# Kernel tuning notes

Measured on AMD Instinct MI355X. Metric: run time of the kernel, lower is better.

The kernel has to match this reference:

```python
import jax, jax.numpy as jnp
import numpy as np

N = 10000
E = 160000
IN_CH, HID, OUT = 14, 128, 4
HEADS = 8
NEG_SLOPE = 0.2


def setup_inputs() -> dict:
    key = jax.random.key(0)
    ks = jax.random.split(key, 16)
    glorot = lambda k, shape: jax.random.normal(k, shape, jnp.float32) * np.sqrt(2.0 / (shape[0] + shape[-1]))
    inp = {
        'x': jax.random.normal(ks[0], (N, IN_CH), jnp.float32),
        'edge_index': jax.random.randint(ks[1], (2, E), 0, N, jnp.int64),
        # layer 1: 14 -> 8 heads x 128, concat
        'W1': glorot(ks[2], (IN_CH, HEADS * HID)),
        'a_src1': glorot(ks[3], (HEADS, HID)),
        'a_dst1': glorot(ks[4], (HEADS, HID)),
        'b1': jnp.zeros((HEADS * HID,), jnp.float32),
        # layer 2: 1024 -> 8 heads x 128, concat
        'W2': glorot(ks[5], (HEADS * HID, HEADS * HID)),
        'a_src2': glorot(ks[6], (HEADS, HID)),
        'a_dst2': glorot(ks[7], (HEADS, HID)),
        'b2': jnp.zeros((HEADS * HID,), jnp.float32),
        # layer 3: 1024 -> 1 head x 4, mean (concat=False)
        'W3': glorot(ks[8], (HEADS * HID, OUT)),
        'a_src3': glorot(ks[9], (1, OUT)),
        'a_dst3': glorot(ks[10], (1, OUT)),
        'b3': jnp.zeros((OUT,), jnp.float32),
    }
    return inp


def gat_conv(x, src, dst, W, a_src, a_dst, b, heads, out_ch, concat):
    n = x.shape[0]
    h = (x @ W).reshape(n, heads, out_ch)                      # [N,H,C]
    al_s = jnp.sum(h * a_src, axis=-1)                         # [N,H]
    al_d = jnp.sum(h * a_dst, axis=-1)                         # [N,H]
    e = al_s[src] + al_d[dst]                                  # [E,H]
    e = jnp.where(e > 0, e, NEG_SLOPE * e)                     # LeakyReLU(0.2)
    # segment softmax over incoming edges of each dst node
    m = jax.ops.segment_max(e, dst, num_segments=n)
    ex = jnp.exp(e - m[dst])
    z = jax.ops.segment_sum(ex, dst, num_segments=n)
    alpha = ex / (z[dst] + 1e-16)                              # [E,H]
    out = jax.ops.segment_sum(h[src] * alpha[:, :, None], dst, num_segments=n)  # [N,H,C]
    out = out.reshape(n, heads * out_ch) if concat else out.mean(axis=1)
    return out + b


def reference(x, edge_index, W1, a_src1, a_dst1, b1, W2, a_src2, a_dst2, b2, W3, a_src3, a_dst3, b3):
    n = x.shape[0]
    # add self-loops (PyG GATConv default)
    loop = jnp.arange(n, dtype=edge_index.dtype)
    src = jnp.concatenate([edge_index[0], loop])
    dst = jnp.concatenate([edge_index[1], loop])
    # dropout layers are identity in eval mode
    h = gat_conv(x, src, dst, W1, a_src1, a_dst1, b1, HEADS, HID, True)
    h = jax.nn.relu(h)
    h = gat_conv(h, src, dst, W2, a_src2, a_dst2, b2, HEADS, HID, True)
    h = jax.nn.relu(h)
    h = gat_conv(h, src, dst, W3, a_src3, a_dst3, b3, 1, OUT, False)
    h = jax.nn.relu(h)
    return h
```

## Files before the change

kernel.cpp:

```cpp
#include <hip/hip_runtime.h>

typedef unsigned short ushort_t;
typedef unsigned int uint32;

#define N_NODES 10000
#define N_EDGES 160000
#define ET (N_NODES + N_EDGES)
#define HT 1024
#define HEADS 8
#define NEG 0.2f

#define O_FLAG     0
#define O_BND      64
#define O_BSUM     192
#define O_COUNTS   512
#define O_OFFS     (O_COUNTS + 40192)
#define O_SSORT    (O_OFFS + 40192)
#define O_ALS1     (O_SSORT + 680192)
#define O_ALD1     (O_ALS1 + 320000)
#define O_ALS2     (O_ALD1 + 320000)
#define O_ALD2     (O_ALS2 + 320000)
#define O_AL3S     O_ALS2
#define O_AL3D     (O_ALS2 + 40192)
#define O_H3       (O_ALS2 + 80384)
#define O_WVEC     (O_ALD2 + 320000)
#define O_W3F      (O_WVEC + 24576)
#define O_S3F      (O_W3F + 16384)
#define O_W2T      (O_S3F + 768)
#define O_BUFA     (O_W2T + 2097152)
#define O_BUFB     (O_BUFA + 20480000)

__device__ __forceinline__ float bf2f(ushort_t u){ return __uint_as_float(((uint32)u) << 16); }
__device__ __forceinline__ ushort_t f2bf(float f){
    uint32 x = __float_as_uint(f);
    return (ushort_t)((x + 0x7fffu + ((x >> 16) & 1u)) >> 16);
}
__device__ __forceinline__ void unpack2(uint32 u, float& lo, float& hi){
    lo = __uint_as_float(u << 16);
    hi = __uint_as_float(u & 0xffff0000u);
}

typedef __bf16 bf16x8 __attribute__((ext_vector_type(8)));
typedef float  f32x4  __attribute__((ext_vector_type(4)));

typedef const __attribute__((address_space(1))) uint32* gas1_u32;
typedef       __attribute__((address_space(3))) uint32* las3_u32;

__device__ __forceinline__ void gload_lds16(const void* g, void* l){
    __builtin_amdgcn_global_load_lds((gas1_u32)g, (las3_u32)l, 16, 0, 0);
}

__device__ __forceinline__ int probe_f32(const uint32* __restrict__ w){
    int cnt = 0;
    for (int i = 0; i < 256; i++){
        uint32 e = (w[i] >> 7) & 0xffu;
        cnt += (e >= 64u && e <= 160u) ? 1 : 0;
    }
    return (cnt > 200) ? 0 : 1;
}
__device__ __forceinline__ int probe_edge64(const int* __restrict__ ei){
    int nz = 0;
    for (int i = 0; i < 128; i++) nz |= ei[2*i + 1];
    return (nz == 0) ? 1 : 0;
}

__device__ __forceinline__ float cvt1(const void* p, int i, int f32){
    return f32 ? ((const float*)p)[i] : bf2f(((const ushort_t*)p)[i]);
}

struct CvtArgs {
    const void* vsrc[6];
    const void* w3src;
    const void* s3src[3];
};

__global__ __launch_bounds__(256) void k_setup(CvtArgs a, const void* __restrict__ W2,
                                               const uint32* __restrict__ w1raw,
                                               const int* __restrict__ eiraw,
                                               int* __restrict__ flags,
                                               float* __restrict__ wvecF, float* __restrict__ W3F,
                                               float* __restrict__ s3F,
                                               int* __restrict__ counts,
                                               float* __restrict__ alS2, float* __restrict__ alD2,
                                               uint32* __restrict__ bnd,
                                               ushort_t* __restrict__ W2T){
    __shared__ ushort_t tile[32][33];
    int b = blockIdx.x, tid = threadIdx.x;
    int f32 = probe_f32(w1raw);
    if (b < 11){
        if (b == 0){
            if (tid < 32) bnd[tid] = 0;
            if (tid == 32) flags[0] = probe_edge64(eiraw);
            if (tid == 33) flags[1] = f32;
        }
        int g = b * 1024 + tid * 4;
        #pragma unroll
        for (int j = 0; j < 4; j++){
            int i = g + j;
            if (i < 6144) wvecF[i] = cvt1(a.vsrc[i >> 10], i & 1023, f32);
            else if (i < 10240) W3F[i - 6144] = cvt1(a.w3src, i - 6144, f32);
            else if (i < 10252){
                int off = i - 10240;
                s3F[(off >> 2) * 16 + (off & 3)] = cvt1(a.s3src[off >> 2], off & 3, f32);
            }
        }
    } else if (b < 21){
        int g = (b - 11) * 1024 + tid * 4;
        #pragma unroll
        for (int j = 0; j < 4; j++) if (g + j < N_NODES) counts[g + j] = 0;
    } else if (b < 178){
        int g = (b - 21) * 1024 + tid * 4;
        if (g < 80000){ *(float4*)(alS2 + g) = make_float4(0,0,0,0); }
        else if (g < 160000){ *(float4*)(alD2 + g - 80000) = make_float4(0,0,0,0); }
    } else {
        int t = b - 178;
        int bx = t & 31, by = t >> 5;
        int cx = tid & 31, ry = (tid >> 5) * 4;
        #pragma unroll
        for (int r = 0; r < 4; r++){
            size_t idx = (size_t)(by*32 + ry + r)*1024 + bx*32 + cx;
            tile[ry + r][cx] = f32 ? f2bf(((const float*)W2)[idx]) : ((const ushort_t*)W2)[idx];
        }
        __syncthreads();
        #pragma unroll
        for (int r = 0; r < 4; r++)
            W2T[(size_t)(bx*32 + ry + r)*1024 + by*32 + cx] = tile[cx][ry + r];
    }
}

__global__ __launch_bounds__(256) void k_exgemm1(const void* __restrict__ ei, const void* __restrict__ x,
                                                 const void* __restrict__ W1, const int* __restrict__ flags,
                                                 const float* __restrict__ wvecF,
                                                 int* __restrict__ counts,
                                                 ushort_t* __restrict__ h1,
                                                 float* __restrict__ alS, float* __restrict__ alD,
                                                 uint32* __restrict__ bnd){
    __shared__ float w1s[14 * HT];
    __shared__ uint32 smax[16];
    int bid = blockIdx.x, tid = threadIdx.x;
    if (bid < 665){
        int i = bid * 256 + tid;
        int is64 = flags[0];
        int d = -1;
        if (i < N_EDGES){
            d = is64 ? (int)((const long long*)ei)[N_EDGES + i] : ((const int*)ei)[N_EDGES + i];
        } else if (i < ET){
            d = i - N_EDGES;
        }
        if (d >= 0) atomicAdd(&counts[d], 1);
        return;
    }
    int gb = bid - 665;
    int f32 = flags[1];
    if (tid < 16) smax[tid] = 0;
    if (f32){
        for (int i = tid * 4; i < 14 * HT; i += 1024)
            *(float4*)(w1s + i) = *(const float4*)((const float*)W1 + i);
    } else {
        for (int i = tid * 4; i < 14 * HT; i += 1024){
            uint2 u = *(const uint2*)((const ushort_t*)W1 + i);
            unpack2(u.x, w1s[i], w1s[i+1]);
            unpack2(u.y, w1s[i+2], w1s[i+3]);
        }
    }
    __syncthreads();
    int c0 = tid * 4;
    float4 sv = *(const float4*)(wvecF + c0);
    float4 dv = *(const float4*)(wvecF + 1024 + c0);
    int head = tid >> 5, l32 = tid & 31;
    #pragma unroll 1
    for (int n = gb; n < N_NODES; n += 512){
        float a0=0.f, a1=0.f, a2=0.f, a3=0.f;
        #pragma unroll
        for (int k = 0; k < 14; k++){
            float xv = f32 ? ((const float*)x)[n*14 + k] : bf2f(((const ushort_t*)x)[n*14 + k]);
            float4 w = *(const float4*)(w1s + k*HT + c0);
            a0 += xv*w.x; a1 += xv*w.y; a2 += xv*w.z; a3 += xv*w.w;
        }
        uint2 o;
        o.x = (uint32)f2bf(a0) | ((uint32)f2bf(a1) << 16);
        o.y = (uint32)f2bf(a2) | ((uint32)f2bf(a3) << 16);
        *(uint2*)(h1 + (size_t)n*HT + c0) = o;
        float h0,h1v,h2,h3v;
        unpack2(o.x, h0, h1v); unpack2(o.y, h2, h3v);
        float s = h0*sv.x + h1v*sv.y + h2*sv.z + h3v*sv.w;
        float d = h0*dv.x + h1v*dv.y + h2*dv.z + h3v*dv.w;
        #pragma unroll
        for (int of = 16; of; of >>= 1){ s += __shfl_xor(s, of, 32); d += __shfl_xor(d, of, 32); }
        if (l32 == 0){
            alS[n*HEADS + head] = s; alD[n*HEADS + head] = d;
            atomicMax(&smax[head],     __float_as_uint(fmaxf(s, 0.f)));
            atomicMax(&smax[8 + head], __float_as_uint(fmaxf(d, 0.f)));
        }
    }
    __syncthreads();
    if (tid < 16) atomicMax(&bnd[tid], smax[tid]);
}

__global__ __launch_bounds__(256) void k_scan_a(const int* __restrict__ counts, int* __restrict__ bsum){
    __shared__ int ws[4];
    int b = blockIdx.x, tid = threadIdx.x;
    int i = b * 256 + tid;
    int v = (i < N_NODES) ? counts[i] : 0;
    int lane = tid & 63, wid = tid >> 6;
    #pragma unroll
    for (int o = 32; o; o >>= 1) v += __shfl_xor(v, o, 64);
    if (lane == 0) ws[wid] = v;
    __syncthreads();
    if (tid == 0) bsum[b] = ws[0] + ws[1] + ws[2] + ws[3];
}

__global__ __launch_bounds__(256) void k_scan_b(int* __restrict__ counts, const int* __restrict__ bsum,
                                                int* __restrict__ offs){
    __shared__ int ws[4];
    int b = blockIdx.x, tid = threadIdx.x;
    int i = b * 256 + tid;
    int v = (i < N_NODES) ? counts[i] : 0;
    int base = 0;
    #pragma unroll 1
    for (int j = 0; j < b; j++) base += bsum[j];
    int lane = tid & 63, wid = tid >> 6;
    int inc = v;
    #pragma unroll
    for (int d = 1; d < 64; d <<= 1){
        int t = __shfl_up(inc, d, 64);
        if (lane >= d) inc += t;
    }
    if (lane == 63) ws[wid] = inc;
    __syncthreads();
    int wpre = 0;
    #pragma unroll
    for (int j = 0; j < 4; j++) if (j < wid) wpre += ws[j];
    int excl = base + wpre + inc - v;
    if (i < N_NODES){ offs[i] = excl; counts[i] = excl; }
    if (i == N_NODES) offs[i] = excl;
}

__global__ __launch_bounds__(256) void k_scatter(const void* __restrict__ ei, const int* __restrict__ flags,
                                                 int* __restrict__ cursors, int* __restrict__ ssort){
    int i = blockIdx.x * 256 + threadIdx.x;
    if (i >= ET) return;
    int is64 = flags[0];
    int s, d;
    if (i < N_EDGES){
        if (is64){
            s = (int)((const long long*)ei)[i];
            d = (int)((const long long*)ei)[N_EDGES + i];
        } else {
            s = ((const int*)ei)[i];
            d = ((const int*)ei)[N_EDGES + i];
        }
    } else { s = i - N_EDGES; d = s; }
    int pos = atomicAdd(&cursors[d], 1);
    ssort[pos] = s;
}

__global__ __launch_bounds__(256) void k_bound(const float* __restrict__ alS2, const float* __restrict__ alD2,
                                               uint32* __restrict__ bnd){
    int g = blockIdx.x * 256 + threadIdx.x;
    int lane = threadIdx.x & 63;
    float ms = 0.f, md = 0.f;
    for (int i = g; i < 80000; i += 10240){ ms = fmaxf(ms, alS2[i]); md = fmaxf(md, alD2[i]); }
    #pragma unroll
    for (int o = 8; o < 64; o <<= 1){
        ms = fmaxf(ms, __shfl_xor(ms, o, 64));
        md = fmaxf(md, __shfl_xor(md, o, 64));
    }
    if (lane < 8){
        atomicMax(&bnd[16 + lane], __float_as_uint(ms));
        atomicMax(&bnd[24 + lane], __float_as_uint(md));
    }
}

__global__ __launch_bounds__(256) void k_gat_agg(const ushort_t* __restrict__ H, const float* __restrict__ alS,
                                                 const float* __restrict__ alD, const uint32* __restrict__ bnd,
                                                 int bo, const int* __restrict__ offs,
                                                 const int* __restrict__ srcs, const float* __restrict__ bias,
                                                 ushort_t* __restrict__ out){
    int tid = threadIdx.x;
    int wv = tid >> 6, lane = tid & 63;
    int n = blockIdx.x * 2 + (wv >> 1);
    int half = wv & 1;
    int beg = offs[n], end = offs[n+1];
    int head = half*4 + (lane >> 4);
    float ad = alD[n*HEADS + head];
    float B = __uint_as_float(bnd[bo + head]) + __uint_as_float(bnd[bo + 8 + head]);

    int ch0 = half*512 + lane*8;
    const ushort_t* Hc = H + ch0;
    float z = 0.f;
    float c0=0.f,c1=0.f,c2=0.f,c3=0.f,c4=0.f,c5=0.f,c6=0.f,c7=0.f;
    for (int c = beg; c < end; c += 64){
        int cn = min(64, end - c);
        int sreg = (lane < cn) ? srcs[c + lane] : 0;
        int j = 0;
        for (; j + 8 <= cn; j += 8){
            int s[8]; uint4 u[8]; float e[8];
            #pragma unroll
            for (int q = 0; q < 8; q++) s[q] = __shfl(sreg, j + q, 64);
            #pragma unroll
            for (int q = 0; q < 8; q++) u[q] = *(const uint4*)(Hc + (size_t)s[q]*HT);
            #pragma unroll
            for (int q = 0; q < 8; q++) e[q] = alS[s[q]*HEADS + head];
            #pragma unroll
            for (int q = 0; q < 8; q++){
                float v = e[q] + ad;
                v = v > 0.f ? v : NEG*v;
                float w = __expf(v - B);
                z += w;
                float f0,f1,f2,f3,f4,f5,f6,f7;
                unpack2(u[q].x,f0,f1); unpack2(u[q].y,f2,f3);
                unpack2(u[q].z,f4,f5); unpack2(u[q].w,f6,f7);
                c0+=w*f0; c1+=w*f1; c2+=w*f2; c3+=w*f3;
                c4+=w*f4; c5+=w*f5; c6+=w*f6; c7+=w*f7;
            }
        }
        for (; j < cn; j++){
            int s0 = __shfl(sreg, j, 64);
            uint4 u0 = *(const uint4*)(Hc + (size_t)s0*HT);
            float v = alS[s0*HEADS + head] + ad;
            v = v > 0.f ? v : NEG*v;
            float w = __expf(v - B);
            z += w;
            float f0,f1,f2,f3,f4,f5,f6,f7;
            unpack2(u0.x,f0,f1); unpack2(u0.y,f2,f3); unpack2(u0.z,f4,f5); unpack2(u0.w,f6,f7);
            c0+=w*f0; c1+=w*f1; c2+=w*f2; c3+=w*f3;
            c4+=w*f4; c5+=w*f5; c6+=w*f6; c7+=w*f7;
        }
    }
    float inv = 1.f / z;
    float4 b0 = *(const float4*)(bias + ch0);
    float4 b1 = *(const float4*)(bias + ch0 + 4);
    c0 = fmaxf(c0*inv + b0.x, 0.f); c1 = fmaxf(c1*inv + b0.y, 0.f);
    c2 = fmaxf(c2*inv + b0.z, 0.f); c3 = fmaxf(c3*inv + b0.w, 0.f);
    c4 = fmaxf(c4*inv + b1.x, 0.f); c5 = fmaxf(c5*inv + b1.y, 0.f);
    c6 = fmaxf(c6*inv + b1.z, 0.f); c7 = fmaxf(c7*inv + b1.w, 0.f);
    uint4 o;
    o.x = (uint32)f2bf(c0) | ((uint32)f2bf(c1) << 16);
    o.y = (uint32)f2bf(c2) | ((uint32)f2bf(c3) << 16);
    o.z = (uint32)f2bf(c4) | ((uint32)f2bf(c5) << 16);
    o.w = (uint32)f2bf(c6) | ((uint32)f2bf(c7) << 16);
    *(uint4*)(out + (size_t)n*HT + ch0) = o;
}

__global__ __launch_bounds__(256) void k_gemm2(const ushort_t* __restrict__ A, const ushort_t* __restrict__ BT,
                                               ushort_t* __restrict__ C,
                                               const float* __restrict__ aS, const float* __restrict__ aD,
                                               float* __restrict__ alS2, float* __restrict__ alD2){
    __shared__ ushort_t lA[128*64];
    __shared__ ushort_t lB[64*64];
    int bn = blockIdx.x, bm = blockIdx.y;
    int tid = threadIdx.x;
    int lane = tid & 63;
    int wave = tid >> 6;
    int wm = wave * 32;
    int lm = lane & 15, kg = lane >> 4;
    int swz = lm & 7;
    f32x4 acc[2][4];
    #pragma unroll
    for (int i = 0; i < 2; i++)
        #pragma unroll
        for (int j = 0; j < 4; j++) acc[i][j] = (f32x4)0.0f;

    int rowA0 = bm * 128, rowB0 = bn * 64;
    for (int k0 = 0; k0 < 1024; k0 += 64){
        #pragma unroll
        for (int it = 0; it < 4; ++it){
            int s = tid + it*256;
            int r = s >> 3, q = s & 7;
            int ra = rowA0 + r; if (ra > N_NODES-1) ra = N_NODES-1;
            gload_lds16(A + (size_t)ra*1024 + k0 + (q ^ (r & 7))*8, lA + s*8);
        }
        #pragma unroll
        for (int it = 0; it < 2; ++it){
            int s = tid + it*256;
            int r = s >> 3, q = s & 7;
            gload_lds16(BT + (size_t)(rowB0 + r)*1024 + k0 + (q ^ (r & 7))*8, lB + s*8);
        }
        __syncthreads();
        #pragma unroll
        for (int kh = 0; kh < 2; kh++){
            bf16x8 af[2], bfr[4];
            int qb = kh*4 + kg;
            int qp = (qb ^ swz) * 8;
            #pragma unroll
            for (int mt = 0; mt < 2; mt++) af[mt]  = *(const bf16x8*)(lA + (wm + mt*16 + lm)*64 + qp);
            #pragma unroll
            for (int nt = 0; nt < 4; nt++) bfr[nt] = *(const bf16x8*)(lB + (nt*16 + lm)*64 + qp);
            #pragma unroll
            for (int mt = 0; mt < 2; mt++)
                #pragma unroll
                for (int nt = 0; nt < 4; nt++)
                    acc[mt][nt] = __builtin_amdgcn_mfma_f32_16x16x32_bf16(af[mt], bfr[nt], acc[mt][nt], 0, 0, 0);
        }
        __syncthreads();
    }
    #pragma unroll
    for (int mt = 0; mt < 2; mt++){
        int row_base = bm*128 + wm + mt*16 + kg*4;
        #pragma unroll
        for (int nt = 0; nt < 4; nt++){
            int col = bn*64 + nt*16 + lm;
            #pragma unroll
            for (int r = 0; r < 4; r++){
                int row = row_base + r;
                if (row < N_NODES) C[(size_t)row*HT + col] = f2bf(acc[mt][nt][r]);
            }
        }
    }
    int head = bn >> 1;
    float as_l[4], ad_l[4];
    #pragma unroll
    for (int nt = 0; nt < 4; nt++){
        as_l[nt] = aS[bn*64 + nt*16 + lm];
        ad_l[nt] = aD[bn*64 + nt*16 + lm];
    }
    #pragma unroll
    for (int mt = 0; mt < 2; mt++){
        #pragma unroll
        for (int r = 0; r < 4; r++){
            float ps = acc[mt][0][r]*as_l[0] + acc[mt][1][r]*as_l[1]
                     + acc[mt][2][r]*as_l[2] + acc[mt][3][r]*as_l[3];
            float pd = acc[mt][0][r]*ad_l[0] + acc[mt][1][r]*ad_l[1]
                     + acc[mt][2][r]*ad_l[2] + acc[mt][3][r]*ad_l[3];
            #pragma unroll
            for (int o = 1; o < 16; o <<= 1){ ps += __shfl_xor(ps, o, 64); pd += __shfl_xor(pd, o, 64); }
            if (lm == 0){
                int row = bm*128 + wm + mt*16 + kg*4 + r;
                if (row < N_NODES){
                    atomicAdd(&alS2[row*HEADS + head], ps);
                    atomicAdd(&alD2[row*HEADS + head], pd);
                }
            }
        }
    }
}

__global__ __launch_bounds__(256) void k_gemm3(const ushort_t* __restrict__ A, const float* __restrict__ W3,
                                               const float* __restrict__ s3,
                                               float* __restrict__ h3, float* __restrict__ al3s, float* __restrict__ al3d){
    int tid = threadIdx.x;
    int lane = tid & 63, wave = tid >> 6;
    int n = blockIdx.x * 4 + wave;
    if (n >= N_NODES) return;
    float4 w3r[16];
    #pragma unroll
    for (int j = 0; j < 16; j++) w3r[j] = ((const float4*)W3)[lane*16 + j];
    const uint4* ap = (const uint4*)(A + (size_t)n*HT + lane*16);
    uint4 u0 = ap[0], u1 = ap[1];
    uint32 uu[8] = {u0.x,u0.y,u0.z,u0.w,u1.x,u1.y,u1.z,u1.w};
    float acc0=0.f, acc1=0.f, acc2=0.f, acc3=0.f;
    #pragma unroll
    for (int p = 0; p < 8; p++){
        float lo, hi;
        unpack2(uu[p], lo, hi);
        float4 wl = w3r[p*2], wh = w3r[p*2+1];
        acc0 += lo*wl.x + hi*wh.x;
        acc1 += lo*wl.y + hi*wh.y;
        acc2 += lo*wl.z + hi*wh.z;
        acc3 += lo*wl.w + hi*wh.w;
    }
    #pragma unroll
    for (int o = 32; o; o >>= 1){
        acc0 += __shfl_xor(acc0, o, 64); acc1 += __shfl_xor(acc1, o, 64);
        acc2 += __shfl_xor(acc2, o, 64); acc3 += __shfl_xor(acc3, o, 64);
    }
    if (lane == 0){
        *(float4*)(h3 + n*4) = make_float4(acc0, acc1, acc2, acc3);
        al3s[n] = acc0*s3[0] + acc1*s3[1] + acc2*s3[2] + acc3*s3[3];
        al3d[n] = acc0*s3[16] + acc1*s3[17] + acc2*s3[18] + acc3*s3[19];
    }
}

__global__ __launch_bounds__(256) void k_gat_agg3(const float* __restrict__ h3, const float* __restrict__ al3s,
                                                  const float* __restrict__ al3d, const int* __restrict__ offs,
                                                  const int* __restrict__ srcs, const float* __restrict__ b3,
                                                  const int* __restrict__ flags, void* __restrict__ out){
    int tid = threadIdx.x;
    int l = tid & 63, wave = tid >> 6;
    int n = blockIdx.x * 4 + wave;
    if (n >= N_NODES) return;
    int beg = offs[n], end = offs[n+1];
    float ad = al3d[n];
    float m = -1e30f;
    for (int e = beg + l; e < end; e += 64){
        float v = al3s[srcs[e]] + ad; v = v > 0.f ? v : NEG*v;
        m = fmaxf(m, v);
    }
    #pragma unroll
    for (int o = 32; o; o >>= 1) m = fmaxf(m, __shfl_xor(m, o, 64));
    float z = 0.f;
    for (int e = beg + l; e < end; e += 64){
        float v = al3s[srcs[e]] + ad; v = v > 0.f ? v : NEG*v;
        z += __expf(v - m);
    }
    #pragma unroll
    for (int o = 32; o; o >>= 1) z += __shfl_xor(z, o, 64);
    float inv = 1.f / (z + 1e-16f);
    float a0=0.f, a1=0.f, a2=0.f, a3=0.f;
    for (int e = beg + l; e < end; e += 64){
        int s = srcs[e];
        float v = al3s[s] + ad; v = v > 0.f ? v : NEG*v;
        float w = __expf(v - m) * inv;
        float4 hv = *(const float4*)(h3 + s*4);
        a0 += w*hv.x; a1 += w*hv.y; a2 += w*hv.z; a3 += w*hv.w;
    }
    #pragma unroll
    for (int o = 32; o; o >>= 1){
        a0 += __shfl_xor(a0, o, 64); a1 += __shfl_xor(a1, o, 64);
        a2 += __shfl_xor(a2, o, 64); a3 += __shfl_xor(a3, o, 64);
    }
    if (l == 0){
        float r0 = fmaxf(a0 + b3[0], 0.f);
        float r1 = fmaxf(a1 + b3[1], 0.f);
        float r2 = fmaxf(a2 + b3[2], 0.f);
        float r3 = fmaxf(a3 + b3[3], 0.f);
        if (flags[1]){
            float* o4 = (float*)out;
            o4[n*4+0]=r0; o4[n*4+1]=r1; o4[n*4+2]=r2; o4[n*4+3]=r3;
        } else {
            ushort_t* o2 = (ushort_t*)out;
            o2[n*4+0]=f2bf(r0); o2[n*4+1]=f2bf(r1); o2[n*4+2]=f2bf(r2); o2[n*4+3]=f2bf(r3);
        }
    }
}

extern "C" void kernel_launch(void* const* d_in, const int* in_sizes, int n_in,
                              void* d_out, int out_size, void* d_ws, size_t ws_size,
                              hipStream_t stream){
    const void* x   = d_in[0];
    const void* ei  = d_in[1];
    const void* W1  = d_in[2];
    const void* W2  = d_in[6];
    const void* W3  = d_in[10];

    char* ws = (char*)d_ws;
    int* flags     = (int*)(ws + O_FLAG);
    uint32* bnd    = (uint32*)(ws + O_BND);
    int* bsum      = (int*)(ws + O_BSUM);
    int* counts    = (int*)(ws + O_COUNTS);
    int* offs      = (int*)(ws + O_OFFS);
    int* ssort     = (int*)(ws + O_SSORT);
    float* alS1    = (float*)(ws + O_ALS1);
    float* alD1    = (float*)(ws + O_ALD1);
    float* alS2    = (float*)(ws + O_ALS2);
    float* alD2    = (float*)(ws + O_ALD2);
    float* al3s    = (float*)(ws + O_AL3S);
    float* al3d    = (float*)(ws + O_AL3D);
    float* h3      = (float*)(ws + O_H3);
    float* wvecF   = (float*)(ws + O_WVEC);
    float* W3F     = (float*)(ws + O_W3F);
    float* s3F     = (float*)(ws + O_S3F);
    ushort_t* W2T  = (ushort_t*)(ws + O_W2T);
    ushort_t* bufA = (ushort_t*)(ws + O_BUFA);
    ushort_t* bufB = (ushort_t*)(ws + O_BUFB);

    const int EB = (ET + 255) / 256;

    CvtArgs ca;
    ca.vsrc[0]=d_in[3];  ca.vsrc[1]=d_in[4];  ca.vsrc[2]=d_in[5];
    ca.vsrc[3]=d_in[7];  ca.vsrc[4]=d_in[8];  ca.vsrc[5]=d_in[9];
    ca.w3src = W3;
    ca.s3src[0]=d_in[11]; ca.s3src[1]=d_in[12]; ca.s3src[2]=d_in[13];

    k_setup<<<1202, 256, 0, stream>>>(ca, W2, (const uint32*)W1, (const int*)ei, flags,
                                      wvecF, W3F, s3F, counts, alS2, alD2, bnd, W2T);
    k_exgemm1<<<1177, 256, 0, stream>>>(ei, x, W1, flags, wvecF, counts, bufA, alS1, alD1, bnd);
    k_scan_a<<<40, 256, 0, stream>>>(counts, bsum);
    k_scan_b<<<40, 256, 0, stream>>>(counts, bsum, offs);
    k_scatter<<<EB, 256, 0, stream>>>(ei, flags, counts, ssort);

    k_gat_agg<<<5000, 256, 0, stream>>>(bufA, alS1, alD1, bnd, 0, offs, ssort, wvecF + 2*1024, bufB);

    k_gemm2<<<dim3(16, 79), 256, 0, stream>>>(bufB, W2T, bufA, wvecF + 3*1024, wvecF + 4*1024, alS2, alD2);
    k_bound<<<40, 256, 0, stream>>>(alS2, alD2, bnd);
    k_gat_agg<<<5000, 256, 0, stream>>>(bufA, alS2, alD2, bnd, 16, offs, ssort, wvecF + 5*1024, bufB);

    k_gemm3<<<2500, 256, 0, stream>>>(bufB, W3F, s3F, h3, al3s, al3d);
    k_gat_agg3<<<2500, 256, 0, stream>>>(h3, al3s, al3d, offs, ssort, s3F + 32, flags, d_out);
}
```

Measured before the change: 335.0 us.

## Shrink setup kernel and merge W2 transpose into the layer-1 mega kernel

The setup kernel is cut down to 12 blocks that only convert the small weight vectors and zero the counts. The W2 transpose and the alS2/alD2 zeroing move into the same launch as the edge counting and the layer-1 GEMM, so that independent work can run concurrently instead of in a serial launch. The W1 shared copy is now stored as bf16 instead of fp32, halving its LDS footprint, which may raise occupancy. The cost is extra unpacking in the inner loop and a heavier, more heterogeneous kernel.

Result: no change. 330.9 us (-1.2%).

```diff
diff --git a/kernel.cpp b/kernel.cpp
--- a/kernel.cpp
+++ b/kernel.cpp
@@ -74,68 +74,49 @@
     const void* s3src[3];
 };
 
-__global__ __launch_bounds__(256) void k_setup(CvtArgs a, const void* __restrict__ W2,
-                                               const uint32* __restrict__ w1raw,
-                                               const int* __restrict__ eiraw,
-                                               int* __restrict__ flags,
-                                               float* __restrict__ wvecF, float* __restrict__ W3F,
-                                               float* __restrict__ s3F,
-                                               int* __restrict__ counts,
-                                               float* __restrict__ alS2, float* __restrict__ alD2,
-                                               uint32* __restrict__ bnd,
-                                               ushort_t* __restrict__ W2T){
-    __shared__ ushort_t tile[32][33];
+__global__ __launch_bounds__(256) void k_pre(CvtArgs a, const uint32* __restrict__ w1raw,
+                                             const int* __restrict__ eiraw,
+                                             int* __restrict__ flags,
+                                             float* __restrict__ wvecF, float* __restrict__ W3F,
+                                             float* __restrict__ s3F,
+                                             int* __restrict__ counts, uint32* __restrict__ bnd){
     int b = blockIdx.x, tid = threadIdx.x;
     int f32 = probe_f32(w1raw);
-    if (b < 11){
-        if (b == 0){
-            if (tid < 32) bnd[tid] = 0;
-            if (tid == 32) flags[0] = probe_edge64(eiraw);
-            if (tid == 33) flags[1] = f32;
-        }
-        int g = b * 1024 + tid * 4;
-        #pragma unroll
-        for (int j = 0; j < 4; j++){
-            int i = g + j;
-            if (i < 6144) wvecF[i] = cvt1(a.vsrc[i >> 10], i & 1023, f32);
-            else if (i < 10240) W3F[i - 6144] = cvt1(a.w3src, i - 6144, f32);
-            else if (i < 10252){
-                int off = i - 10240;
-                s3F[(off >> 2) * 16 + (off & 3)] = cvt1(a.s3src[off >> 2], off & 3, f32);
-            }
-        }
-    } else if (b < 21){
-        int g = (b - 11) * 1024 + tid * 4;
-        #pragma unroll
-        for (int j = 0; j < 4; j++) if (g + j < N_NODES) counts[g + j] = 0;
-    } else if (b < 178){
-        int g = (b - 21) * 1024 + tid * 4;
-        if (g < 80000){ *(float4*)(alS2 + g) = make_float4(0,0,0,0); }
-        else if (g < 160000){ *(float4*)(alD2 + g - 80000) = make_float4(0,0,0,0); }
+    if (b == 0){
+        if (tid < 32) bnd[tid] = 0;
+        if (tid == 32) flags[0] = probe_edge64(eiraw);
+        if (tid == 33) flags[1] = f32;
+        if (tid >= 64 && tid < 76){
+            int off = tid - 64;
+            s3F[(off >> 2) * 16 + (off & 3)] = cvt1(a.s3src[off >> 2], off & 3, f32);
+        }
+    } else if (b <= 6){
+        int g = tid * 4;
+        #pragma unroll
+        for (int j = 0; j < 4; j++) wvecF[(b-1)*1024 + g + j] = cvt1(a.vsrc[b-1], g + j, f32);
+    } else if (b <= 10){
+        int g = (b - 7) * 1024 + tid * 4;
+        #pragma unroll
+        for (int j = 0; j < 4; j++) W3F[g + j] = cvt1(a.w3src, g + j, f32);
     } else {
-        int t = b - 178;
-        int bx = t & 31, by = t >> 5;
-        int cx = tid & 31, ry = (tid >> 5) * 4;
-        #pragma unroll
-        for (int r = 0; r < 4; r++){
-            size_t idx = (size_t)(by*32 + ry + r)*1024 + bx*32 + cx;
-            tile[ry + r][cx] = f32 ? f2bf(((const float*)W2)[idx]) : ((const ushort_t*)W2)[idx];
-        }
-        __syncthreads();
-        #pragma unroll
-        for (int r = 0; r < 4; r++)
-            W2T[(size_t)(bx*32 + ry + r)*1024 + by*32 + cx] = tile[cx][ry + r];
-    }
-}
-
-__global__ __launch_bounds__(256) void k_exgemm1(const void* __restrict__ ei, const void* __restrict__ x,
-                                                 const void* __restrict__ W1, const int* __restrict__ flags,
-                                                 const float* __restrict__ wvecF,
-                                                 int* __restrict__ counts,
-                                                 ushort_t* __restrict__ h1,
-                                                 float* __restrict__ alS, float* __restrict__ alD,
-                                                 uint32* __restrict__ bnd){
-    __shared__ float w1s[14 * HT];
+        for (int i = tid * 4; i < N_NODES; i += 1024){
+            #pragma unroll
+            for (int j = 0; j < 4; j++) if (i + j < N_NODES) counts[i + j] = 0;
+        }
+    }
+}
+
+__global__ __launch_bounds__(256) void k_mega1(const void* __restrict__ ei, const void* __restrict__ x,
+                                               const void* __restrict__ W1, const void* __restrict__ W2,
+                                               const int* __restrict__ flags,
+                                               const float* __restrict__ wvecF,
+                                               int* __restrict__ counts,
+                                               ushort_t* __restrict__ h1,
+                                               float* __restrict__ alS, float* __restrict__ alD,
+                                               uint32* __restrict__ bnd,
+                                               ushort_t* __restrict__ W2T,
+                                               float* __restrict__ alS2, float* __restrict__ alD2){
+    __shared__ ushort_t lsh[14336];
     __shared__ uint32 smax[16];
     int bid = blockIdx.x, tid = threadIdx.x;
     if (bid < 665){
@@ -150,51 +131,77 @@
         if (d >= 0) atomicAdd(&counts[d], 1);
         return;
     }
-    int gb = bid - 665;
-    int f32 = flags[1];
-    if (tid < 16) smax[tid] = 0;
-    if (f32){
-        for (int i = tid * 4; i < 14 * HT; i += 1024)
-            *(float4*)(w1s + i) = *(const float4*)((const float*)W1 + i);
-    } else {
-        for (int i = tid * 4; i < 14 * HT; i += 1024){
-            uint2 u = *(const uint2*)((const ushort_t*)W1 + i);
-            unpack2(u.x, w1s[i], w1s[i+1]);
-            unpack2(u.y, w1s[i+2], w1s[i+3]);
-        }
-    }
-    __syncthreads();
-    int c0 = tid * 4;
-    float4 sv = *(const float4*)(wvecF + c0);
-    float4 dv = *(const float4*)(wvecF + 1024 + c0);
-    int head = tid >> 5, l32 = tid & 31;
-    #pragma unroll 1
-    for (int n = gb; n < N_NODES; n += 512){
-        float a0=0.f, a1=0.f, a2=0.f, a3=0.f;
-        #pragma unroll
-        for (int k = 0; k < 14; k++){
-            float xv = f32 ? ((const float*)x)[n*14 + k] : bf2f(((const ushort_t*)x)[n*14 + k]);
-            float4 w = *(const float4*)(w1s + k*HT + c0);
-            a0 += xv*w.x; a1 += xv*w.y; a2 += xv*w.z; a3 += xv*w.w;
-        }
-        uint2 o;
-        o.x = (uint32)f2bf(a0) | ((uint32)f2bf(a1) << 16);
-        o.y = (uint32)f2bf(a2) | ((uint32)f2bf(a3) << 16);
-        *(uint2*)(h1 + (size_t)n*HT + c0) = o;
-        float h0,h1v,h2,h3v;
-        unpack2(o.x, h0, h1v); unpack2(o.y, h2, h3v);
-        float s = h0*sv.x + h1v*sv.y + h2*sv.z + h3v*sv.w;
-        float d = h0*dv.x + h1v*dv.y + h2*dv.z + h3v*dv.w;
-        #pragma unroll
-        for (int of = 16; of; of >>= 1){ s += __shfl_xor(s, of, 32); d += __shfl_xor(d, of, 32); }
-        if (l32 == 0){
-            alS[n*HEADS + head] = s; alD[n*HEADS + head] = d;
-            atomicMax(&smax[head],     __float_as_uint(fmaxf(s, 0.f)));
-            atomicMax(&smax[8 + head], __float_as_uint(fmaxf(d, 0.f)));
-        }
-    }
-    __syncthreads();
-    if (tid < 16) atomicMax(&bnd[tid], smax[tid]);
+    if (bid < 1177){
+        int gb = bid - 665;
+        int f32 = flags[1];
+        if (tid < 16) smax[tid] = 0;
+        if (f32){
+            for (int i = tid; i < 14336; i += 256) lsh[i] = f2bf(((const float*)W1)[i]);
+        } else {
+            for (int i = tid * 8; i < 14336; i += 2048)
+                *(uint4*)(lsh + i) = *(const uint4*)((const ushort_t*)W1 + i);
+        }
+        __syncthreads();
+        int c0 = tid * 4;
+        float4 sv = *(const float4*)(wvecF + c0);
+        float4 dv = *(const float4*)(wvecF + 1024 + c0);
+        int head = tid >> 5, l32 = tid & 31;
+        #pragma unroll 1
+        for (int n = gb; n < N_NODES; n += 512){
+            float a0=0.f, a1=0.f, a2=0.f, a3=0.f;
+            #pragma unroll
+            for (int k = 0; k < 14; k++){
+                float xv = f32 ? ((const float*)x)[n*14 + k] : bf2f(((const ushort_t*)x)[n*14 + k]);
+                uint2 u = *(const uint2*)(lsh + k*HT + c0);
+                float w0,w1,w2,w3;
+                unpack2(u.x, w0, w1); unpack2(u.y, w2, w3);
+                a0 += xv*w0; a1 += xv*w1; a2 += xv*w2; a3 += xv*w3;
+            }
+            uint2 o;
+            o.x = (uint32)f2bf(a0) | ((uint32)f2bf(a1) << 16);
+            o.y = (uint32)f2bf(a2) | ((uint32)f2bf(a3) << 16);
+            *(uint2*)(h1 + (size_t)n*HT + c0) = o;
+            float h0,h1v,h2,h3v;
+            unpack2(o.x, h0, h1v); unpack2(o.y, h2, h3v);
+            float s = h0*sv.x + h1v*sv.y + h2*sv.z + h3v*sv.w;
+            float d = h0*dv.x + h1v*dv.y + h2*dv.z + h3v*dv.w;
+            #pragma unroll
+            for (int of = 16; of; of >>= 1){ s += __shfl_xor(s, of, 32); d += __shfl_xor(d, of, 32); }
+            if (l32 == 0){
+                alS[n*HEADS + head] = s; alD[n*HEADS + head] = d;
+                atomicMax(&smax[head],     __float_as_uint(fmaxf(s, 0.f)));
+                atomicMax(&smax[8 + head], __float_as_uint(fmaxf(d, 0.f)));
+            }
+        }
+        __syncthreads();
+        if (tid < 16) atomicMax(&bnd[tid], smax[tid]);
+        return;
+    }
+    if (bid < 1689){
+        int f32 = flags[1];
+        ushort_t (*tile)[33] = (ushort_t (*)[33])lsh;
+        int cx = tid & 31, ry = (tid >> 5) * 4;
+        int t2 = (bid - 1177) * 2;
+        #pragma unroll 1
+        for (int tt = 0; tt < 2; tt++){
+            int t = t2 + tt;
+            int bx = t & 31, by = t >> 5;
+            __syncthreads();
+            #pragma unroll
+            for (int r = 0; r < 4; r++){
+                size_t idx = (size_t)(by*32 + ry + r)*1024 + bx*32 + cx;
+                tile[ry + r][cx] = f32 ? f2bf(((const float*)W2)[idx]) : ((const ushort_t*)W2)[idx];
+            }
+            __syncthreads();
+            #pragma unroll
+            for (int r = 0; r < 4; r++)
+                W2T[(size_t)(bx*32 + ry + r)*1024 + by*32 + cx] = tile[cx][ry + r];
+        }
+        return;
+    }
+    int g = (bid - 1689) * 1024 + tid * 4;
+    if (g < 80000){ *(float4*)(alS2 + g) = make_float4(0,0,0,0); }
+    else if (g < 160000){ *(float4*)(alD2 + g - 80000) = make_float4(0,0,0,0); }
 }
 
 __global__ __launch_bounds__(256) void k_scan_a(const int* __restrict__ counts, int* __restrict__ bsum){
@@ -563,9 +570,10 @@
     ca.w3src = W3;
     ca.s3src[0]=d_in[11]; ca.s3src[1]=d_in[12]; ca.s3src[2]=d_in[13];
 
-    k_setup<<<1202, 256, 0, stream>>>(ca, W2, (const uint32*)W1, (const int*)ei, flags,
-                                      wvecF, W3F, s3F, counts, alS2, alD2, bnd, W2T);
-    k_exgemm1<<<1177, 256, 0, stream>>>(ei, x, W1, flags, wvecF, counts, bufA, alS1, alD1, bnd);
+    k_pre<<<12, 256, 0, stream>>>(ca, (const uint32*)W1, (const int*)ei, flags,
+                                  wvecF, W3F, s3F, counts, bnd);
+    k_mega1<<<1846, 256, 0, stream>>>(ei, x, W1, W2, flags, wvecF, counts,
+                                      bufA, alS1, alD1, bnd, W2T, alS2, alD2);
     k_scan_a<<<40, 256, 0, stream>>>(counts, bsum);
     k_scan_b<<<40, 256, 0, stream>>>(counts, bsum, offs);
     k_scatter<<<EB, 256, 0, stream>>>(ei, flags, counts, ssort);
```
